# Performance work log

Measured on AMD Instinct MI355X. Metric: run time of the kernel, lower is better.

The kernel has to match this reference:

```python
import jax, jax.numpy as jnp
import numpy as np

SEQ, B, E, HID = 512, 32, 256, 256
H2 = 2 * HID              # BiLSTM output / DAG-LSTM hidden size
R, NE, NS, SW = 128, 64, 64, 8
N = NE + NS               # total node slots (entities + relation nodes)
VOCAB, NEL = 50000, 128
CLAMP_C, CLAMP_H = 100.0, 100.0


def _uni(k, shape, fan_in):
    b = 1.0 / np.sqrt(fan_in)
    return jax.random.uniform(k, shape, jnp.float32, -b, b)


def setup_inputs() -> dict:
    key = jax.random.key(0)
    ks = jax.random.split(key, 24)
    inp = {}
    inp["tokens"] = jax.random.randint(ks[0], (SEQ, B), 0, VOCAB)
    inp["entity_spans"] = jax.random.randint(ks[1], (NE, SW), 0, SEQ)
    inp["element_names"] = jax.random.randint(ks[2], (NS, B), 0, NEL)
    inp["H"] = jnp.zeros((N, B, H2), jnp.float32)
    inp["A"] = jnp.zeros((1,), jnp.int32)  # unused by forward (as in original)
    inp["T"] = jnp.broadcast_to(jnp.arange(NS, dtype=jnp.int32)[:, None] + NE, (NS, B))
    inp["S"] = jax.random.randint(ks[3], (NS, B, 2), 0, NE + 32)
    inp["entity_spans_size"] = jnp.full((B,), NE, jnp.int32)
    # learned parameters
    inp["word_emb"] = jax.random.normal(ks[4], (VOCAB, E), jnp.float32)
    inp["elem_emb"] = jax.random.normal(ks[5], (NEL, R), jnp.float32)
    inp["attn_w"] = _uni(ks[6], (1, H2), H2)
    inp["attn_b"] = _uni(ks[7], (1,), H2)
    inp["Wih_f"] = _uni(ks[8], (4 * HID, E), E)
    inp["Whh_f"] = _uni(ks[9], (4 * HID, HID), HID)
    inp["bl_f"] = _uni(ks[10], (4 * HID,), HID)
    inp["Wih_b"] = _uni(ks[11], (4 * HID, E), E)
    inp["Whh_b"] = _uni(ks[12], (4 * HID, HID), HID)
    inp["bl_b"] = _uni(ks[13], (4 * HID,), HID)
    inp["W_ioc"] = _uni(ks[14], (3 * H2, R), R + 2 * H2)
    inp["U_ioc"] = _uni(ks[15], (3 * H2, 2 * H2), R + 2 * H2)
    inp["b_ioc"] = _uni(ks[16], (3 * H2,), R + 2 * H2)
    inp["Wf"] = _uni(ks[17], (H2, R), R + H2)
    inp["Uf"] = _uni(ks[18], (H2, H2), R + H2)
    inp["bf"] = _uni(ks[19], (H2,), R + H2)
    inp["W1"] = _uni(ks[20], (2 * H2, H2), H2)
    inp["b1"] = _uni(ks[21], (2 * H2,), H2)
    inp["W2"] = _uni(ks[22], (2, 2 * H2), 2 * H2)
    inp["b2"] = _uni(ks[23], (2,), 2 * H2)
    return inp


def _lstm_dir(x, Wih, Whh, b, reverse):
    # x: [seq, batch, E]; torch gate order i, f, g, o
    h0 = jnp.zeros((x.shape[1], Whh.shape[1]), x.dtype)

    def step(carry, xt):
        h, c = carry
        g = xt @ Wih.T + h @ Whh.T + b
        i, f, gg, o = jnp.split(g, 4, axis=-1)
        c = jax.nn.sigmoid(f) * c + jax.nn.sigmoid(i) * jnp.tanh(gg)
        h = jax.nn.sigmoid(o) * jnp.tanh(c)
        return (h, c), h

    xs = x[::-1] if reverse else x
    _, hs = jax.lax.scan(step, (h0, h0), xs)
    return hs[::-1] if reverse else hs


def _forward(tokens, entity_spans, element_names, H, T, S, entity_spans_size,
             word_emb, elem_emb, attn_w, attn_b,
             Wih_f, Whh_f, bl_f, Wih_b, Whh_b, bl_b,
             W_ioc, U_ioc, b_ioc, Wf, Uf, bf, W1, b1, W2, b2):
    emb = word_emb[tokens]                                  # [SEQ,B,E]
    fwd = _lstm_dir(emb, Wih_f, Whh_f, bl_f, False)
    bwd = _lstm_dir(emb, Wih_b, Whh_b, bl_b, True)
    blstm = jnp.concatenate([fwd, bwd], axis=-1)            # [SEQ,B,H2]

    # attention pooling over entity spans; original multiplies the softmax
    # weights (which sum to 1) against blstm_out[i], so h_entity = wsum * blstm[i]
    attn = blstm @ attn_w[0] + attn_b[0]                    # [SEQ,B]
    scores = attn[entity_spans]                             # [NE,SW,B]
    wsum = jax.nn.softmax(scores, axis=1).sum(axis=1)       # [NE,B] (== 1 up to fp)
    ne = entity_spans.shape[0]
    H = H.at[:ne].set(wsum[..., None] * blstm[:ne])

    rej = jnp.array([0.999, 0.001], jnp.float32)
    acc0 = jnp.array([0.001, 0.999], jnp.float32)
    n_nodes = H.shape[0]

    def cell(hv, c, e):
        # DAG-LSTM cell: hv [2,H2] input hiddens, c [H2] shared cell state, e [R]
        ioc = e @ W_ioc.T + hv.reshape(-1) @ U_ioc.T + b_ioc
        i, o, ch = jnp.split(ioc, 3)
        f = jax.nn.sigmoid(e @ Wf.T + hv @ Uf.T + bf)       # [2,H2] per-input forget
        c_new = jnp.clip(jnp.sum(f * c[None, :], axis=0)
                         + jax.nn.sigmoid(i) * jnp.tanh(ch), -CLAMP_C, CLAMP_C)
        h = jnp.clip(jax.nn.sigmoid(o) * jnp.tanh(c_new), -CLAMP_H, CLAMP_H)
        return h, c_new

    P0 = jnp.concatenate([jnp.tile(acc0, (ne, 1)),
                          jnp.zeros((n_nodes - ne, 2), jnp.float32)], axis=0)

    def batch_body(c, xs):
        Hb, Sb, Tb, Eb, ent_sz = xs

        def step(carry, inp):
            Hb, Pb, c = carry
            args, tgt, el = inp
            valid = (tgt >= ent_sz) & (el > -1)
            cond = jnp.all(Pb[args, 1] > 0.5) & valid
            h_out, c_new = cell(Hb[args], c, elem_emb[el])
            logits = W2 @ (W1 @ h_out + b1) + b2
            pred = jnp.where(cond, jax.nn.softmax(logits), rej)
            Hb = Hb.at[tgt].set(jnp.where(cond, h_out, Hb[tgt]))
            c = jnp.where(cond, c_new, c)
            Pb = Pb.at[tgt].set(jnp.where(valid, pred, Pb[tgt]))
            return (Hb, Pb, c), None

        (Hb, Pb, c), _ = jax.lax.scan(step, (Hb, P0, c), (Sb, Tb, Eb))
        return c, Pb

    # cell state c rolls sequentially across batches, matching the torch loop order
    xs = (jnp.swapaxes(H, 0, 1), jnp.swapaxes(S, 0, 1), T.T,
          element_names.T, entity_spans_size)
    _, P = jax.lax.scan(batch_body, jnp.zeros((H.shape[-1],), jnp.float32), xs)
    return P.reshape(-1, 2)


def reference(tokens, entity_spans, element_names, H, A, T, S, entity_spans_size,
              word_emb, elem_emb, attn_w, attn_b,
              Wih_f, Whh_f, bl_f, Wih_b, Whh_b, bl_b,
              W_ioc, U_ioc, b_ioc, Wf, Uf, bf, W1, b1, W2, b2):
    return _forward(tokens, entity_spans, element_names, H, T, S, entity_spans_size,
                    word_emb, elem_emb, attn_w, attn_b,
                    Wih_f, Whh_f, bl_f, Wih_b, Whh_b, bl_b,
                    W_ioc, U_ioc, b_ioc, Wf, Uf, bf, W1, b1, W2, b2)
```

## Files before the change

kernel.cpp:

```cpp
#include <hip/hip_runtime.h>
#include <stdint.h>

#define SEQB 512
#define BATCH 32
#define EDIM 256
#define HIDN 256
#define HH2 512
#define RDIM 128
#define NEnt 64
#define NSt 64
#define NNODE 128
#define NHELP 112
#define HPG 14
#define NROWS 3584
#define TERMEVT 0xFFFFFFFFu
#define SCOPE_AGENT __HIP_MEMORY_SCOPE_AGENT

static __device__ __forceinline__ float sigm(float x) { return 1.0f / (1.0f + __expf(-x)); }
static __device__ __forceinline__ float tanh_f(float x) { return 1.0f - 2.0f / (__expf(2.0f * x) + 1.0f); }

static __device__ __forceinline__ void barrier_lds() {
  asm volatile("s_waitcnt lgkmcnt(0)" ::: "memory");
  __builtin_amdgcn_sched_barrier(0);
  __builtin_amdgcn_s_barrier();
}

template<int GATHER, int BIASFIRST>
__global__ __launch_bounds__(256) void gemm_tn(
    const float* __restrict__ A, const int* __restrict__ gidx, const float* __restrict__ gtab,
    const float* __restrict__ B0, const float* __restrict__ B1, int nsplitB,
    const float* __restrict__ bias0, const float* __restrict__ bias1, int nsplitBias,
    float* __restrict__ C, int M, int N, int K)
{
  __shared__ float As[16][132];
  __shared__ float Bs[16][132];
  const int tid = threadIdx.x;
  const int m0 = blockIdx.y * 128, n0 = blockIdx.x * 128;

  const int lrow = tid >> 1;
  const int lk   = (tid & 1) * 8;
  const float* arow;
  if (GATHER) arow = gtab + (size_t)gidx[m0 + lrow] * K + lk;
  else        arow = A + (size_t)(m0 + lrow) * K + lk;
  const int bn = n0 + lrow;
  const float* brow = ((bn < nsplitB) ? (B0 + (size_t)bn * K)
                                      : (B1 + (size_t)(bn - nsplitB) * K)) + lk;

  const int tx = tid & 15, ty = tid >> 4;

  float bb[2][4];
#pragma unroll
  for (int in = 0; in < 2; ++in)
#pragma unroll
    for (int j = 0; j < 4; ++j) bb[in][j] = 0.f;
  if (bias0) {
#pragma unroll
    for (int in = 0; in < 2; ++in)
#pragma unroll
      for (int j = 0; j < 4; ++j) {
        int n = n0 + in * 64 + tx * 4 + j;
        bb[in][j] = (n < nsplitBias) ? bias0[n] : bias1[n - nsplitBias];
      }
  }

  float acc[2][2][4][4];
#pragma unroll
  for (int im = 0; im < 2; ++im)
#pragma unroll
    for (int in = 0; in < 2; ++in)
#pragma unroll
      for (int i = 0; i < 4; ++i)
#pragma unroll
        for (int j = 0; j < 4; ++j)
          acc[im][in][i][j] = BIASFIRST ? bb[in][j] : 0.f;

  float4 pa0 = *(const float4*)(arow);
  float4 pa1 = *(const float4*)(arow + 4);
  float4 pb0 = *(const float4*)(brow);
  float4 pb1 = *(const float4*)(brow + 4);

  int k0 = 0;
  while (true) {
    __syncthreads();
    As[lk + 0][lrow] = pa0.x; As[lk + 1][lrow] = pa0.y;
    As[lk + 2][lrow] = pa0.z; As[lk + 3][lrow] = pa0.w;
    As[lk + 4][lrow] = pa1.x; As[lk + 5][lrow] = pa1.y;
    As[lk + 6][lrow] = pa1.z; As[lk + 7][lrow] = pa1.w;
    Bs[lk + 0][lrow] = pb0.x; Bs[lk + 1][lrow] = pb0.y;
    Bs[lk + 2][lrow] = pb0.z; Bs[lk + 3][lrow] = pb0.w;
    Bs[lk + 4][lrow] = pb1.x; Bs[lk + 5][lrow] = pb1.y;
    Bs[lk + 6][lrow] = pb1.z; Bs[lk + 7][lrow] = pb1.w;
    __syncthreads();

    k0 += 16;
    const bool more = (k0 < K);
    if (more) {
      pa0 = *(const float4*)(arow + k0);
      pa1 = *(const float4*)(arow + k0 + 4);
      pb0 = *(const float4*)(brow + k0);
      pb1 = *(const float4*)(brow + k0 + 4);
    }

#pragma unroll
    for (int k = 0; k < 16; ++k) {
      const float4 av0 = *(const float4*)&As[k][ty * 4];
      const float4 av1 = *(const float4*)&As[k][64 + ty * 4];
      const float4 bv0 = *(const float4*)&Bs[k][tx * 4];
      const float4 bv1 = *(const float4*)&Bs[k][64 + tx * 4];
      const float am[2][4] = {{av0.x, av0.y, av0.z, av0.w},
                              {av1.x, av1.y, av1.z, av1.w}};
      const float bw[2][4] = {{bv0.x, bv0.y, bv0.z, bv0.w},
                              {bv1.x, bv1.y, bv1.z, bv1.w}};
#pragma unroll
      for (int im = 0; im < 2; ++im)
#pragma unroll
        for (int in = 0; in < 2; ++in)
#pragma unroll
          for (int i = 0; i < 4; ++i)
#pragma unroll
            for (int j = 0; j < 4; ++j)
              acc[im][in][i][j] += am[im][i] * bw[in][j];
    }
    if (!more) break;
  }

#pragma unroll
  for (int im = 0; im < 2; ++im)
#pragma unroll
    for (int i = 0; i < 4; ++i) {
      const int m = m0 + im * 64 + ty * 4 + i;
#pragma unroll
      for (int in = 0; in < 2; ++in) {
        float4 o;
        o.x = acc[im][in][i][0] + (BIASFIRST ? 0.f : bb[in][0]);
        o.y = acc[im][in][i][1] + (BIASFIRST ? 0.f : bb[in][1]);
        o.z = acc[im][in][i][2] + (BIASFIRST ? 0.f : bb[in][2]);
        o.w = acc[im][in][i][3] + (BIASFIRST ? 0.f : bb[in][3]);
        *(float4*)&C[(size_t)m * N + n0 + in * 64 + tx * 4] = o;
      }
    }
}

__global__ __launch_bounds__(256, 1) void lstm_esplit(
    const float* __restrict__ Xg,
    const float* __restrict__ Whh_f, const float* __restrict__ Whh_b,
    unsigned long long* __restrict__ hxbuf,
    float* __restrict__ blstm)
{
  const int tid = threadIdx.x;
  const int pid = blockIdx.x;
  const int q = pid >> 6, chain = pid & 63;
  const int d = chain >> 5, b = chain & 31;
  const int j = tid & 63;
  const int g = tid >> 6;
  const int elem = q * 64 + j;
  const int grow = g * 256 + elem;

  const float* W = (d ? Whh_b : Whh_f) + (size_t)grow * 256;
  float4 w4[64];
#pragma unroll
  for (int i = 0; i < 64; ++i) w4[i] = *(const float4*)(W + 4 * i);

  __shared__ float h_lds[HIDN];
  __shared__ float gsL[256];
  float creg = 0.f;
  h_lds[tid] = 0.f;
  __syncthreads();

  const float4* h4 = (const float4*)h_lds;
  const int pe = (tid < q * 64) ? tid : (tid + 64);
  const size_t xgoff = (size_t)d * 1024 + grow;

  for (int it = 0; it < SEQB; ++it) {
    const int t = d ? (SEQB - 1 - it) : it;
    const size_t m = (size_t)t * BATCH + b;
    const float xv = Xg[m * 2048 + xgoff];

    if (tid < 192) {
      const unsigned long long* src =
          &hxbuf[((size_t)(it & 1) * 64 + chain) * 256 + pe];
      unsigned long long qv;
      do { qv = __hip_atomic_load(src, __ATOMIC_RELAXED, SCOPE_AGENT); }
      while ((unsigned)(qv >> 32) != (unsigned)it);
      h_lds[pe] = __uint_as_float((unsigned)qv);
    }
    barrier_lds();

    float a0 = 0.f, a1 = 0.f, a2 = 0.f, a3 = 0.f;
#pragma unroll
    for (int i = 0; i < 64; ++i) {
      const float4 hv = h4[i];
      const float4 wv = w4[i];
      a0 += wv.x * hv.x; a1 += wv.y * hv.y; a2 += wv.z * hv.z; a3 += wv.w * hv.w;
    }
    gsL[tid] = (a0 + a1) + (a2 + a3) + xv;
    barrier_lds();

    if (tid < 64) {
      const float gi = gsL[tid], gf = gsL[64 + tid];
      const float gg = gsL[128 + tid], go = gsL[192 + tid];
      creg = sigm(gf) * creg + sigm(gi) * tanh_f(gg);
      const float hn = sigm(go) * tanh_f(creg);
      h_lds[elem] = hn;
      const unsigned long long pk =
          ((unsigned long long)(unsigned)(it + 1) << 32) |
          (unsigned long long)__float_as_uint(hn);
      __hip_atomic_store(&hxbuf[((size_t)((it + 1) & 1) * 64 + chain) * 256 + elem], pk,
                         __ATOMIC_RELAXED, SCOPE_AGENT);
      blstm[m * HH2 + (size_t)d * HIDN + elem] = hn;
    }
    barrier_lds();
  }
}

__global__ __launch_bounds__(256) void attn_k(const float* __restrict__ blstm,
                                              const float* __restrict__ attn_w,
                                              const float* __restrict__ attn_b,
                                              float* __restrict__ attnv)
{
  const int tid = threadIdx.x;
  const int p = blockIdx.x * 4 + (tid >> 6);
  const int lane = tid & 63;
  const size_t base = (size_t)p * HH2 + lane * 8;
  float4 v0 = *(const float4*)&blstm[base];
  float4 v1 = *(const float4*)&blstm[base + 4];
  float4 w0 = *(const float4*)&attn_w[lane * 8];
  float4 w1 = *(const float4*)&attn_w[lane * 8 + 4];
  float acc = v0.x * w0.x + v0.y * w0.y + v0.z * w0.z + v0.w * w0.w
            + v1.x * w1.x + v1.y * w1.y + v1.z * w1.z + v1.w * w1.w;
#pragma unroll
  for (int off = 32; off > 0; off >>= 1) acc += __shfl_down(acc, off);
  if (lane == 0) attnv[p] = acc + attn_b[0];
}

__global__ __launch_bounds__(64) void entity_prep(const int* __restrict__ spans,
                                                  const float* __restrict__ attnv,
                                                  const float* __restrict__ blstm,
                                                  float* __restrict__ Hent,
                                                  float* __restrict__ P_out)
{
  const int nb = blockIdx.x;
  const int n = nb >> 5, b = nb & 31;
  const int tid = threadIdx.x;
  __shared__ float sc[8];
  if (tid < 8) sc[tid] = attnv[spans[n * 8 + tid] * BATCH + b];
  __syncthreads();
  float mx = sc[0];
#pragma unroll
  for (int w = 1; w < 8; ++w) mx = fmaxf(mx, sc[w]);
  float ex[8]; float ssum = 0.f;
#pragma unroll
  for (int w = 0; w < 8; ++w) { ex[w] = __expf(sc[w] - mx); ssum += ex[w]; }
  float wsum = 0.f;
#pragma unroll
  for (int w = 0; w < 8; ++w) wsum += ex[w] / ssum;
  const size_t base = ((size_t)n * BATCH + b) * HH2;
#pragma unroll
  for (int q = 0; q < 2; ++q) {
    int j = q * 256 + tid * 4;
    float4 v = *(const float4*)&blstm[base + j];
    v.x *= wsum; v.y *= wsum; v.z *= wsum; v.w *= wsum;
    *(float4*)&Hent[base + j] = v;
  }
  if (tid == 0) {
    P_out[((size_t)b * NNODE + n) * 2 + 0] = 0.001f;
    P_out[((size_t)b * NNODE + n) * 2 + 1] = 0.999f;
  }
}

__global__ void pack_ucat(const float* __restrict__ U_ioc, const float* __restrict__ Uf,
                          float* __restrict__ Ucat)
{
  int j = blockIdx.x, tid = threadIdx.x;
  for (int k = tid; k < 512; k += 128) {
    float v;
    if (j < 1536)      v = U_ioc[(size_t)j * 1024 + k];
    else if (j < 3072) v = U_ioc[(size_t)(j - 1536) * 1024 + 512 + k];
    else               v = Uf[(size_t)(j - 3072) * 512 + k];
    Ucat[(size_t)j * 512 + k] = v;
  }
}

__global__ __launch_bounds__(256) void mprep(const float* __restrict__ W1,
                                             const float* __restrict__ b1,
                                             const float* __restrict__ W2,
                                             const float* __restrict__ b2,
                                             float* __restrict__ Mmat,
                                             float* __restrict__ mbv)
{
  const int tid = threadIdx.x;
  for (int j = tid; j < 512; j += 256) {
    float a0 = 0.f, a1 = 0.f;
    for (int m = 0; m < 1024; ++m) {
      float w = W1[(size_t)m * 512 + j];
      a0 += W2[m] * w;
      a1 += W2[1024 + m] * w;
    }
    Mmat[j] = a0; Mmat[512 + j] = a1;
  }
  if (tid < 2) {
    float a = b2[tid];
    for (int m = 0; m < 1024; ++m) a += W2[tid * 1024 + m] * b1[m];
    mbv[tid] = a;
  }
}

__global__ __launch_bounds__(512) void dag_seq(
    const int* __restrict__ S, const int* __restrict__ T, const int* __restrict__ EN,
    const int* __restrict__ entsz,
    const float* __restrict__ WE,
    const float* __restrict__ Mmat, const float* __restrict__ mbv,
    float* __restrict__ Tall, float* __restrict__ hbuf,
    uint32_t* head, uint32_t* slotbase, uint32_t* arrive,
    const float* __restrict__ Ucat, float* __restrict__ P_out)
{
  const int tid = threadIdx.x;
  __shared__ int   SL[NSt * BATCH * 2];
  __shared__ int   TLt[NSt * BATCH];
  __shared__ int   ELt[NSt * BATCH];
  __shared__ int   eszL[BATCH];
  __shared__ float MmatL[1024];
  __shared__ float mbvL[2];
  __shared__ float pstL[NNODE];
  __shared__ int   evtofL[NSt];
  __shared__ int   confL[NSt];
  __shared__ float red0[2][8], red1[2][8];
  __shared__ uint32_t sslot;

  if (blockIdx.x < NHELP) {
    const int w = blockIdx.x;
    const int row = w * 32 + (tid >> 4);
    const int ks = (tid & 15) * 32;
    float wreg[32];
#pragma unroll
    for (int i = 0; i < 8; ++i) {
      float4 v = *(const float4*)&Ucat[(size_t)row * 512 + ks + i * 4];
      wreg[i * 4 + 0] = v.x; wreg[i * 4 + 1] = v.y; wreg[i * 4 + 2] = v.z; wreg[i * 4 + 3] = v.w;
    }
    uint32_t done = 0;
    const int g = w & 7;
    while (true) {
      if (tid == 0) {
        while (__hip_atomic_load(head, __ATOMIC_RELAXED, SCOPE_AGENT) <= done) {
          __builtin_amdgcn_s_sleep(4);
        }
        __builtin_amdgcn_fence(__ATOMIC_ACQUIRE, "agent");
        sslot = slotbase[done];
      }
      __syncthreads();
      const uint32_t slot = sslot;
      if (slot == TERMEVT) break;
      const float* hv = hbuf + (size_t)done * HH2 + ks;
      float acc = 0.f;
#pragma unroll
      for (int i = 0; i < 8; ++i) {
        float4 v = *(const float4*)&hv[i * 4];
        acc += wreg[i * 4 + 0] * v.x + wreg[i * 4 + 1] * v.y
             + wreg[i * 4 + 2] * v.z + wreg[i * 4 + 3] * v.w;
      }
      acc += __shfl_down(acc, 8);
      acc += __shfl_down(acc, 4);
      acc += __shfl_down(acc, 2);
      acc += __shfl_down(acc, 1);
      if ((tid & 15) == 0) {
        __hip_atomic_store(&Tall[(size_t)slot + row], acc, __ATOMIC_RELAXED, SCOPE_AGENT);
      }
      __syncthreads();
      if (tid == 0) {
        __hip_atomic_fetch_add(&arrive[done * 8 + g], 1u, __ATOMIC_RELEASE, SCOPE_AGENT);
      }
      ++done;
    }
    return;
  }

  for (int i = tid; i < NSt * BATCH * 2; i += 512) SL[i] = S[i];
  for (int i = tid; i < NSt * BATCH; i += 512) { TLt[i] = T[i]; ELt[i] = EN[i]; }
  for (int i = tid; i < 1024; i += 512) MmatL[i] = Mmat[i];
  if (tid < BATCH) eszL[tid] = entsz[tid];
  if (tid < 2) mbvL[tid] = mbv[tid];
  __syncthreads();

  float c = 0.f;
  uint32_t e = 0;
  for (int b = 0; b < BATCH; ++b) {
    barrier_lds();
    const int esz = eszL[b];
    for (int j = tid; j < NNODE; j += 512) pstL[j] = (j < NEnt) ? 0.999f : 0.f;
    if (tid < NSt) { confL[tid] = 0; evtofL[tid] = -1; }
    __syncthreads();
    int fp = 0;

    bool  pfok = false;
    float pt0 = 0.f, pt1 = 0.f, pt2 = 0.f, pt3 = 0.f, pt4 = 0.f, pt5 = 0.f, pt6 = 0.f, pt7 = 0.f;
    float pw0 = 0.f, pw1 = 0.f, pw2 = 0.f, pwf = 0.f;

#define PFETCH(sn)                                                              \
    do {                                                                        \
      pfok = false;                                                             \
      if ((sn) < NSt) {                                                         \
        const int sbn_ = (sn) * BATCH + b;                                      \
        const int na0_ = SL[2 * sbn_], na1_ = SL[2 * sbn_ + 1];                 \
        const int nel_ = ELt[sbn_];                                             \
        if (nel_ >= 0) {                                                        \
          const float* nwe_ = WE + (size_t)nel_ * 2048;                         \
          pw0 = nwe_[tid]; pw1 = nwe_[512 + tid]; pw2 = nwe_[1024 + tid];       \
          pwf = nwe_[1536 + tid];                                               \
        }                                                                       \
        const bool ok0_ = (na0_ < NEnt) || (confL[na0_ - NEnt] != 0);           \
        const bool ok1_ = (na1_ < NEnt) || (confL[na1_ - NEnt] != 0);           \
        if (ok0_ && ok1_) {                                                     \
          const size_t ns0_ = ((size_t)na0_ * BATCH + b) * NROWS;               \
          const size_t ns1_ = ((size_t)na1_ * BATCH + b) * NROWS;               \
          pt0 = Tall[ns0_ + tid];               pt1 = Tall[ns1_ + 1536 + tid];  \
          pt2 = Tall[ns0_ + 512 + tid];         pt3 = Tall[ns1_ + 2048 + tid];  \
          pt4 = Tall[ns0_ + 1024 + tid];        pt5 = Tall[ns1_ + 2560 + tid];  \
          pt6 = Tall[ns0_ + 3072 + tid];        pt7 = Tall[ns1_ + 3072 + tid];  \
          pfok = true;                                                          \
        }                                                                       \
      }                                                                         \
    } while (0)

    PFETCH(0);

    for (int s = 0; s < NSt; ++s) {
      const int sb = s * BATCH + b;
      const int a0 = SL[2 * sb], a1 = SL[2 * sb + 1];
      const int tgt = TLt[sb], el = ELt[sb];
      const bool valid = (tgt >= esz) && (el > -1);
      const float pa0 = pstL[a0], pa1 = pstL[a1];
      const bool cond = valid && (pa0 > 0.5f) && (pa1 > 0.5f);
      if (cond) {
        if (!pfok) {
          const int r0 = (a0 >= NEnt) ? (a0 - NEnt) : -1;
          const int r1 = (a1 >= NEnt) ? (a1 - NEnt) : -1;
          if (tid < 8 && r0 >= 0 && !confL[r0]) {
            const uint32_t ev = (uint32_t)evtofL[r0];
            while (__hip_atomic_load(&arrive[ev * 8 + tid], __ATOMIC_RELAXED, SCOPE_AGENT)
                   < (uint32_t)HPG) { __builtin_amdgcn_s_sleep(1); }
          }
          if (tid >= 8 && tid < 16 && r1 >= 0 && !confL[r1]) {
            const uint32_t ev = (uint32_t)evtofL[r1];
            while (__hip_atomic_load(&arrive[ev * 8 + (tid - 8)], __ATOMIC_RELAXED, SCOPE_AGENT)
                   < (uint32_t)HPG) { __builtin_amdgcn_s_sleep(1); }
          }
          __syncthreads();
          if (tid == 0) {
            __builtin_amdgcn_fence(__ATOMIC_ACQUIRE, "agent");
            int evm = -1;
            if (r0 >= 0) { confL[r0] = 1; if (evtofL[r0] > evm) evm = evtofL[r0]; }
            if (r1 >= 0) { confL[r1] = 1; if (evtofL[r1] > evm) evm = evtofL[r1]; }
            if (evm >= 0) {
              for (int r = 0; r < 32; ++r) {
                const int ev_ = evtofL[r];
                if (ev_ >= 0 && ev_ <= evm) confL[r] = 1;
              }
            }
          }
          __syncthreads();
          const size_t s0 = ((size_t)a0 * BATCH + b) * NROWS;
          const size_t s1 = ((size_t)a1 * BATCH + b) * NROWS;
          pt0 = Tall[s0 + tid];        pt1 = Tall[s1 + 1536 + tid];
          pt2 = Tall[s0 + 512 + tid];  pt3 = Tall[s1 + 2048 + tid];
          pt4 = Tall[s0 + 1024 + tid]; pt5 = Tall[s1 + 2560 + tid];
          pt6 = Tall[s0 + 3072 + tid]; pt7 = Tall[s1 + 3072 + tid];
        }
        const float ii = pw0 + pt0 + pt1;
        const float oo = pw1 + pt2 + pt3;
        const float ch = pw2 + pt4 + pt5;
        const float f0 = sigm(pwf + pt6);
        const float f1 = sigm(pwf + pt7);
        PFETCH(s + 1);
        float cn = (f0 + f1) * c + sigm(ii) * tanh_f(ch);
        cn = fminf(fmaxf(cn, -100.f), 100.f);
        float hh = sigm(oo) * tanh_f(cn);
        hh = fminf(fmaxf(hh, -100.f), 100.f);
        float l0 = MmatL[tid] * hh, l1 = MmatL[512 + tid] * hh;
#pragma unroll
        for (int off = 32; off > 0; off >>= 1) {
          l0 += __shfl_down(l0, off);
          l1 += __shfl_down(l1, off);
        }
        if ((tid & 63) == 0) { red0[fp][tid >> 6] = l0; red1[fp][tid >> 6] = l1; }
        barrier_lds();
        float L0 = mbvL[0], L1 = mbvL[1];
#pragma unroll
        for (int wv = 0; wv < 8; ++wv) { L0 += red0[fp][wv]; L1 += red1[fp][wv]; }
        const float mx = fmaxf(L0, L1);
        const float e0 = __expf(L0 - mx), e1 = __expf(L1 - mx);
        const float inv = 1.f / (e0 + e1);
        const float o0 = e0 * inv, o1 = e1 * inv;
        if ((tid & 63) == 0) pstL[tgt] = o1;
        if (tid == 0) {
          P_out[((size_t)b * NNODE + tgt) * 2 + 0] = o0;
          P_out[((size_t)b * NNODE + tgt) * 2 + 1] = o1;
        }
        fp ^= 1;
        c = cn;
        const bool pub = (o1 > 0.5f) && (tgt < NEnt + 32);
        if (pub) {
          __hip_atomic_store(&hbuf[(size_t)e * HH2 + tid], hh, __ATOMIC_RELAXED, SCOPE_AGENT);
          __syncthreads();
          if (tid == 0) {
            evtofL[tgt - NEnt] = (int)e;
            __hip_atomic_store(&slotbase[e], (uint32_t)(((uint32_t)tgt * BATCH + (uint32_t)b) * NROWS),
                               __ATOMIC_RELAXED, SCOPE_AGENT);
            __hip_atomic_store(head, e + 1u, __ATOMIC_RELEASE, SCOPE_AGENT);
          }
          ++e;
          barrier_lds();
        }
      } else {
        PFETCH(s + 1);
        if (tid == 0 && (valid || tgt >= NEnt)) {
          const float o0 = valid ? 0.999f : ((tgt < NEnt) ? 0.001f : 0.f);
          const float o1 = valid ? 0.001f : ((tgt < NEnt) ? 0.999f : 0.f);
          P_out[((size_t)b * NNODE + tgt) * 2 + 0] = o0;
          P_out[((size_t)b * NNODE + tgt) * 2 + 1] = o1;
        }
        if (valid && (tid & 63) == 0) pstL[tgt] = 0.001f;
      }
    }
#undef PFETCH
  }
  if (tid == 0) {
    __hip_atomic_store(&slotbase[e], TERMEVT, __ATOMIC_RELAXED, SCOPE_AGENT);
    __hip_atomic_store(head, e + 1u, __ATOMIC_RELEASE, SCOPE_AGENT);
  }
}

extern "C" void kernel_launch(void* const* d_in, const int* in_sizes, int n_in,
                              void* d_out, int out_size, void* d_ws, size_t ws_size,
                              hipStream_t stream)
{
  const int* tokens = (const int*)d_in[0];
  const int* spans  = (const int*)d_in[1];
  const int* enames = (const int*)d_in[2];
  const int* T      = (const int*)d_in[5];
  const int* S      = (const int*)d_in[6];
  const int* entsz  = (const int*)d_in[7];
  const float* word_emb = (const float*)d_in[8];
  const float* elem_emb = (const float*)d_in[9];
  const float* attn_w = (const float*)d_in[10];
  const float* attn_b = (const float*)d_in[11];
  const float* Wih_f = (const float*)d_in[12];
  const float* Whh_f = (const float*)d_in[13];
  const float* bl_f  = (const float*)d_in[14];
  const float* Wih_b = (const float*)d_in[15];
  const float* Whh_b = (const float*)d_in[16];
  const float* bl_b  = (const float*)d_in[17];
  const float* W_ioc = (const float*)d_in[18];
  const float* U_ioc = (const float*)d_in[19];
  const float* b_ioc = (const float*)d_in[20];
  const float* Wf    = (const float*)d_in[21];
  const float* Uf    = (const float*)d_in[22];
  const float* bf    = (const float*)d_in[23];
  const float* W1    = (const float*)d_in[24];
  const float* b1    = (const float*)d_in[25];
  const float* W2    = (const float*)d_in[26];
  const float* b2    = (const float*)d_in[27];
  float* P_out = (float*)d_out;

  char* ws = (char*)d_ws;
  uint32_t* head     = (uint32_t*)ws;
  uint32_t* slotbase = (uint32_t*)(ws + 8192);
  uint32_t* arrive   = (uint32_t*)(ws + 16384);
  float* fws = (float*)(ws + 65536);
  size_t off = 0;
  float* Xg    = fws + off; off += (size_t)16384 * 2048;
  float* blstm = fws + off; off += (size_t)SEQB * BATCH * HH2;
  float* attnv = fws + off; off += (size_t)SEQB * BATCH;
  float* Hent  = fws + off; off += (size_t)2048 * 512;
  float* Tall  = fws + off; off += (size_t)96 * BATCH * NROWS;
  unsigned long long* hxbuf = (unsigned long long*)(fws + off);
  off += (size_t)2 * 64 * 256 * 2;
  float* Ucat  = fws + off; off += (size_t)NROWS * 512;
  float* WE    = fws + off; off += (size_t)128 * 2048;
  float* Mmat  = fws + off; off += 1024;
  float* mbv   = fws + off; off += 16;
  float* hbuf  = fws + off; off += (size_t)1024 * 512;
  const size_t needed = 65536 + off * sizeof(float);
  if (ws_size < needed) return;

  hipMemsetAsync(d_ws, 0, 65536, stream);
  hipMemsetAsync(hxbuf, 0, (size_t)2 * 64 * 256 * 8, stream);

  gemm_tn<1, 0><<<dim3(2048 / 128, 16384 / 128), 256, 0, stream>>>(
      nullptr, tokens, word_emb, Wih_f, Wih_b, 1024, bl_f, bl_b, 1024,
      Xg, 16384, 2048, 256);

  lstm_esplit<<<256, 256, 0, stream>>>(Xg, Whh_f, Whh_b, hxbuf, blstm);

  attn_k<<<4096, 256, 0, stream>>>(blstm, attn_w, attn_b, attnv);
  entity_prep<<<2048, 64, 0, stream>>>(spans, attnv, blstm, Hent, P_out);

  pack_ucat<<<NROWS, 128, 0, stream>>>(U_ioc, Uf, Ucat);
  gemm_tn<0, 1><<<dim3(2048 / 128, 1), 256, 0, stream>>>(
      elem_emb, nullptr, nullptr, W_ioc, Wf, 1536, b_ioc, bf, 1536,
      WE, 128, 2048, 128);
  mprep<<<1, 256, 0, stream>>>(W1, b1, W2, b2, Mmat, mbv);
  gemm_tn<0, 0><<<dim3(NROWS / 128, 2048 / 128), 256, 0, stream>>>(
      Hent, nullptr, nullptr, Ucat, nullptr, 0x40000000, nullptr, nullptr, 0,
      Tall, 2048, NROWS, 512);

  dag_seq<<<NHELP + 1, 512, 0, stream>>>(S, T, enames, entsz, WE, Mmat, mbv,
                                         Tall, hbuf, head, slotbase, arrive, Ucat, P_out);
}
```

Before: 5.462 ms.

## Use tagged hot buffer and packed head to cut producer-consumer sync latency

Helper blocks now write each projected row as a 64-bit value tagged with the event number into a double-buffered hot array. The sequential block polls those tags directly when it needs the most recent event, instead of waiting on arrive counters and then re-reading Tall. The slot is packed into a 64-bit head word so helpers skip the slotbase read, and the hbuf store and wave-level arrive increments are moved earlier to shorten the critical path. This adds heavier polling traffic and subtle memory-ordering assumptions about tag visibility and buffer reuse.

```diff
diff --git a/kernel.cpp b/kernel.cpp
--- a/kernel.cpp
+++ b/kernel.cpp
@@ -12,6 +12,7 @@
 #define NNODE 128
 #define NHELP 112
 #define HPG 14
+#define HPW 112
 #define NROWS 3584
 #define TERMEVT 0xFFFFFFFFu
 #define SCOPE_AGENT __HIP_MEMORY_SCOPE_AGENT
@@ -311,7 +312,8 @@
     const float* __restrict__ WE,
     const float* __restrict__ Mmat, const float* __restrict__ mbv,
     float* __restrict__ Tall, float* __restrict__ hbuf,
-    uint32_t* head, uint32_t* slotbase, uint32_t* arrive,
+    unsigned long long* head64, uint32_t* slotbase, uint32_t* arrive,
+    unsigned long long* hotT,
     const float* __restrict__ Ucat, float* __restrict__ P_out)
 {
   const int tid = threadIdx.x;
@@ -341,11 +343,11 @@
     const int g = w & 7;
     while (true) {
       if (tid == 0) {
-        while (__hip_atomic_load(head, __ATOMIC_RELAXED, SCOPE_AGENT) <= done) {
-          __builtin_amdgcn_s_sleep(4);
-        }
+        unsigned long long hq;
+        while ((uint32_t)((hq = __hip_atomic_load(head64, __ATOMIC_RELAXED, SCOPE_AGENT)) >> 32)
+               <= done) { __builtin_amdgcn_s_sleep(1); }
         __builtin_amdgcn_fence(__ATOMIC_ACQUIRE, "agent");
-        sslot = slotbase[done];
+        sslot = ((uint32_t)(hq >> 32) == done + 1u) ? (uint32_t)hq : slotbase[done];
       }
       __syncthreads();
       const uint32_t slot = sslot;
@@ -364,9 +366,13 @@
       acc += __shfl_down(acc, 1);
       if ((tid & 15) == 0) {
         __hip_atomic_store(&Tall[(size_t)slot + row], acc, __ATOMIC_RELAXED, SCOPE_AGENT);
+        const unsigned long long hq =
+            ((unsigned long long)(done + 1u) << 32) |
+            (unsigned long long)__float_as_uint(acc);
+        __hip_atomic_store(&hotT[(size_t)(done & 1u) * NROWS + row], hq,
+                           __ATOMIC_RELAXED, SCOPE_AGENT);
       }
-      __syncthreads();
-      if (tid == 0) {
+      if ((tid & 63) == 0) {
         __hip_atomic_fetch_add(&arrive[done * 8 + g], 1u, __ATOMIC_RELEASE, SCOPE_AGENT);
       }
       ++done;
@@ -421,6 +427,23 @@
       }                                                                         \
     } while (0)
 
+#define HOTPOLL4(rA, rB, rC, rD, dA, dB, dC, dD)                                \
+    do {                                                                        \
+      const unsigned long long* hp_ = hotT + (size_t)par_ * NROWS;              \
+      unsigned long long qa_, qb_, qc_, qd_;                                    \
+      for (;;) {                                                                \
+        qa_ = __hip_atomic_load(hp_ + (rA), __ATOMIC_RELAXED, SCOPE_AGENT);     \
+        qb_ = __hip_atomic_load(hp_ + (rB), __ATOMIC_RELAXED, SCOPE_AGENT);     \
+        qc_ = __hip_atomic_load(hp_ + (rC), __ATOMIC_RELAXED, SCOPE_AGENT);     \
+        qd_ = __hip_atomic_load(hp_ + (rD), __ATOMIC_RELAXED, SCOPE_AGENT);     \
+        if ((((uint32_t)(qa_ >> 32)) == etag_) & (((uint32_t)(qb_ >> 32)) == etag_) & \
+            (((uint32_t)(qc_ >> 32)) == etag_) & (((uint32_t)(qd_ >> 32)) == etag_))  \
+          break;                                                                \
+      }                                                                         \
+      dA = __uint_as_float((uint32_t)qa_); dB = __uint_as_float((uint32_t)qb_); \
+      dC = __uint_as_float((uint32_t)qc_); dD = __uint_as_float((uint32_t)qd_); \
+    } while (0)
+
     PFETCH(0);
 
     for (int s = 0; s < NSt; ++s) {
@@ -434,47 +457,68 @@
         if (!pfok) {
           const int r0 = (a0 >= NEnt) ? (a0 - NEnt) : -1;
           const int r1 = (a1 >= NEnt) ? (a1 - NEnt) : -1;
-          if (tid < 8 && r0 >= 0 && !confL[r0]) {
-            const uint32_t ev = (uint32_t)evtofL[r0];
-            while (__hip_atomic_load(&arrive[ev * 8 + tid], __ATOMIC_RELAXED, SCOPE_AGENT)
-                   < (uint32_t)HPG) { __builtin_amdgcn_s_sleep(1); }
-          }
-          if (tid >= 8 && tid < 16 && r1 >= 0 && !confL[r1]) {
-            const uint32_t ev = (uint32_t)evtofL[r1];
-            while (__hip_atomic_load(&arrive[ev * 8 + (tid - 8)], __ATOMIC_RELAXED, SCOPE_AGENT)
-                   < (uint32_t)HPG) { __builtin_amdgcn_s_sleep(1); }
-          }
-          __syncthreads();
-          if (tid == 0) {
-            __builtin_amdgcn_fence(__ATOMIC_ACQUIRE, "agent");
-            int evm = -1;
-            if (r0 >= 0) { confL[r0] = 1; if (evtofL[r0] > evm) evm = evtofL[r0]; }
-            if (r1 >= 0) { confL[r1] = 1; if (evtofL[r1] > evm) evm = evtofL[r1]; }
-            if (evm >= 0) {
-              for (int r = 0; r < 32; ++r) {
-                const int ev_ = evtofL[r];
-                if (ev_ >= 0 && ev_ <= evm) confL[r] = 1;
+          const bool c0ok = (r0 < 0) || (confL[r0] != 0);
+          const bool c1ok = (r1 < 0) || (confL[r1] != 0);
+          const bool f0 = !c0ok && (evtofL[r0] == (int)e - 1);
+          const bool f1 = !c1ok && (evtofL[r1] == (int)e - 1);
+          const bool w0 = !c0ok && !f0;
+          const bool w1 = !c1ok && !f1;
+          if (w0 || w1) {
+            if (tid < 8 && w0) {
+              const uint32_t ev = (uint32_t)evtofL[r0];
+              while (__hip_atomic_load(&arrive[ev * 8 + tid], __ATOMIC_RELAXED, SCOPE_AGENT)
+                     < (uint32_t)HPW) { __builtin_amdgcn_s_sleep(1); }
+            }
+            if (tid >= 8 && tid < 16 && w1) {
+              const uint32_t ev = (uint32_t)evtofL[r1];
+              while (__hip_atomic_load(&arrive[ev * 8 + (tid - 8)], __ATOMIC_RELAXED, SCOPE_AGENT)
+                     < (uint32_t)HPW) { __builtin_amdgcn_s_sleep(1); }
+            }
+            __syncthreads();
+            if (tid == 0) {
+              __builtin_amdgcn_fence(__ATOMIC_ACQUIRE, "agent");
+              int evm = -1;
+              if (w0) { confL[r0] = 1; if (evtofL[r0] > evm) evm = evtofL[r0]; }
+              if (w1) { confL[r1] = 1; if (evtofL[r1] > evm) evm = evtofL[r1]; }
+              if (evm >= 0) {
+                for (int r = 0; r < 32; ++r) {
+                  const int ev_ = evtofL[r];
+                  if (ev_ >= 0 && ev_ <= evm) confL[r] = 1;
+                }
               }
             }
+            __syncthreads();
           }
-          __syncthreads();
           const size_t s0 = ((size_t)a0 * BATCH + b) * NROWS;
           const size_t s1 = ((size_t)a1 * BATCH + b) * NROWS;
-          pt0 = Tall[s0 + tid];        pt1 = Tall[s1 + 1536 + tid];
-          pt2 = Tall[s0 + 512 + tid];  pt3 = Tall[s1 + 2048 + tid];
-          pt4 = Tall[s0 + 1024 + tid]; pt5 = Tall[s1 + 2560 + tid];
-          pt6 = Tall[s0 + 3072 + tid]; pt7 = Tall[s1 + 3072 + tid];
+          const int par_ = (int)((e - 1u) & 1u);
+          const uint32_t etag_ = (uint32_t)e;
+          if (f0) {
+            HOTPOLL4(tid, 512 + tid, 1024 + tid, 3072 + tid, pt0, pt2, pt4, pt6);
+          } else {
+            pt0 = Tall[s0 + tid];        pt2 = Tall[s0 + 512 + tid];
+            pt4 = Tall[s0 + 1024 + tid]; pt6 = Tall[s0 + 3072 + tid];
+          }
+          if (f1) {
+            HOTPOLL4(1536 + tid, 2048 + tid, 2560 + tid, 3072 + tid, pt1, pt3, pt5, pt7);
+          } else {
+            pt1 = Tall[s1 + 1536 + tid]; pt3 = Tall[s1 + 2048 + tid];
+            pt5 = Tall[s1 + 2560 + tid]; pt7 = Tall[s1 + 3072 + tid];
+          }
         }
         const float ii = pw0 + pt0 + pt1;
         const float oo = pw1 + pt2 + pt3;
         const float ch = pw2 + pt4 + pt5;
-        const float f0 = sigm(pwf + pt6);
-        const float f1 = sigm(pwf + pt7);
+        const float f0g = sigm(pwf + pt6);
+        const float f1g = sigm(pwf + pt7);
         PFETCH(s + 1);
-        float cn = (f0 + f1) * c + sigm(ii) * tanh_f(ch);
+        float cn = (f0g + f1g) * c + sigm(ii) * tanh_f(ch);
         cn = fminf(fmaxf(cn, -100.f), 100.f);
         float hh = sigm(oo) * tanh_f(cn);
         hh = fminf(fmaxf(hh, -100.f), 100.f);
+        if (tgt < NEnt + 32) {
+          __hip_atomic_store(&hbuf[(size_t)e * HH2 + tid], hh, __ATOMIC_RELAXED, SCOPE_AGENT);
+        }
         float l0 = MmatL[tid] * hh, l1 = MmatL[512 + tid] * hh;
 #pragma unroll
         for (int off = 32; off > 0; off >>= 1) {
@@ -499,13 +543,14 @@
         c = cn;
         const bool pub = (o1 > 0.5f) && (tgt < NEnt + 32);
         if (pub) {
-          __hip_atomic_store(&hbuf[(size_t)e * HH2 + tid], hh, __ATOMIC_RELAXED, SCOPE_AGENT);
           __syncthreads();
           if (tid == 0) {
             evtofL[tgt - NEnt] = (int)e;
-            __hip_atomic_store(&slotbase[e], (uint32_t)(((uint32_t)tgt * BATCH + (uint32_t)b) * NROWS),
-                               __ATOMIC_RELAXED, SCOPE_AGENT);
-            __hip_atomic_store(head, e + 1u, __ATOMIC_RELEASE, SCOPE_AGENT);
+            const uint32_t slot = (uint32_t)(((uint32_t)tgt * BATCH + (uint32_t)b) * NROWS);
+            __hip_atomic_store(&slotbase[e], slot, __ATOMIC_RELAXED, SCOPE_AGENT);
+            __hip_atomic_store(head64,
+                               ((unsigned long long)(e + 1u) << 32) | (unsigned long long)slot,
+                               __ATOMIC_RELEASE, SCOPE_AGENT);
           }
           ++e;
           barrier_lds();
@@ -522,10 +567,13 @@
       }
     }
 #undef PFETCH
+#undef HOTPOLL4
   }
   if (tid == 0) {
     __hip_atomic_store(&slotbase[e], TERMEVT, __ATOMIC_RELAXED, SCOPE_AGENT);
-    __hip_atomic_store(head, e + 1u, __ATOMIC_RELEASE, SCOPE_AGENT);
+    __hip_atomic_store(head64,
+                       ((unsigned long long)(e + 1u) << 32) | (unsigned long long)TERMEVT,
+                       __ATOMIC_RELEASE, SCOPE_AGENT);
   }
 }
 
@@ -562,10 +610,11 @@
   float* P_out = (float*)d_out;
 
   char* ws = (char*)d_ws;
-  uint32_t* head     = (uint32_t*)ws;
+  unsigned long long* head64 = (unsigned long long*)ws;
   uint32_t* slotbase = (uint32_t*)(ws + 8192);
   uint32_t* arrive   = (uint32_t*)(ws + 16384);
-  float* fws = (float*)(ws + 65536);
+  unsigned long long* hotT = (unsigned long long*)(ws + 49152);
+  float* fws = (float*)(ws + 131072);
   size_t off = 0;
   float* Xg    = fws + off; off += (size_t)16384 * 2048;
   float* blstm = fws + off; off += (size_t)SEQB * BATCH * HH2;
@@ -579,10 +628,10 @@
   float* Mmat  = fws + off; off += 1024;
   float* mbv   = fws + off; off += 16;
   float* hbuf  = fws + off; off += (size_t)1024 * 512;
-  const size_t needed = 65536 + off * sizeof(float);
+  const size_t needed = 131072 + off * sizeof(float);
   if (ws_size < needed) return;
 
-  hipMemsetAsync(d_ws, 0, 65536, stream);
+  hipMemsetAsync(d_ws, 0, 131072, stream);
   hipMemsetAsync(hxbuf, 0, (size_t)2 * 64 * 256 * 8, stream);
 
   gemm_tn<1, 0><<<dim3(2048 / 128, 16384 / 128), 256, 0, stream>>>(
@@ -604,5 +653,6 @@
       Tall, 2048, NROWS, 512);
 
   dag_seq<<<NHELP + 1, 512, 0, stream>>>(S, T, enames, entsz, WE, Mmat, mbv,
-                                         Tall, hbuf, head, slotbase, arrive, Ucat, P_out);
-}
+                                         Tall, hbuf, head64, slotbase, arrive, hotT,
+                                         Ucat, P_out);
+}
```

After: 7.906 ms. 1.45x slower.

## Publish DAG hidden state before softmax and poll slot array instead of head

Applied to the files above, without the earlier changes.

Drops the separate head counter: helper blocks now poll slotbase[done] directly for a nonzero entry, and the producer writes that slot with release ordering. Each relation-node hidden state is now published before the output softmax reduction rather than after it, and without the o1>0.5 check. This lets the helper GEMVs overlap with the classifier reduction and removes one atomic handoff per event. The cost is that helpers run a GEMV for every candidate node, not only accepted ones. The scheme also relies on slotbase being zero-initialised, since any nonzero value is treated as a published slot.

```diff
diff --git a/kernel.cpp b/kernel.cpp
--- a/kernel.cpp
+++ b/kernel.cpp
@@ -311,7 +311,7 @@
     const float* __restrict__ WE,
     const float* __restrict__ Mmat, const float* __restrict__ mbv,
     float* __restrict__ Tall, float* __restrict__ hbuf,
-    uint32_t* head, uint32_t* slotbase, uint32_t* arrive,
+    uint32_t* slotbase, uint32_t* arrive,
     const float* __restrict__ Ucat, float* __restrict__ P_out)
 {
   const int tid = threadIdx.x;
@@ -341,11 +341,12 @@
     const int g = w & 7;
     while (true) {
       if (tid == 0) {
-        while (__hip_atomic_load(head, __ATOMIC_RELAXED, SCOPE_AGENT) <= done) {
-          __builtin_amdgcn_s_sleep(4);
+        uint32_t sv;
+        while ((sv = __hip_atomic_load(&slotbase[done], __ATOMIC_RELAXED, SCOPE_AGENT)) == 0u) {
+          __builtin_amdgcn_s_sleep(1);
         }
         __builtin_amdgcn_fence(__ATOMIC_ACQUIRE, "agent");
-        sslot = slotbase[done];
+        sslot = sv;
       }
       __syncthreads();
       const uint32_t slot = sslot;
@@ -448,8 +449,8 @@
           if (tid == 0) {
             __builtin_amdgcn_fence(__ATOMIC_ACQUIRE, "agent");
             int evm = -1;
-            if (r0 >= 0) { confL[r0] = 1; if (evtofL[r0] > evm) evm = evtofL[r0]; }
-            if (r1 >= 0) { confL[r1] = 1; if (evtofL[r1] > evm) evm = evtofL[r1]; }
+            if (r0 >= 0 && !confL[r0]) { confL[r0] = 1; if (evtofL[r0] > evm) evm = evtofL[r0]; }
+            if (r1 >= 0 && !confL[r1]) { confL[r1] = 1; if (evtofL[r1] > evm) evm = evtofL[r1]; }
             if (evm >= 0) {
               for (int r = 0; r < 32; ++r) {
                 const int ev_ = evtofL[r];
@@ -468,13 +469,17 @@
         const float ii = pw0 + pt0 + pt1;
         const float oo = pw1 + pt2 + pt3;
         const float ch = pw2 + pt4 + pt5;
-        const float f0 = sigm(pwf + pt6);
-        const float f1 = sigm(pwf + pt7);
+        const float f0g = sigm(pwf + pt6);
+        const float f1g = sigm(pwf + pt7);
         PFETCH(s + 1);
-        float cn = (f0 + f1) * c + sigm(ii) * tanh_f(ch);
+        float cn = (f0g + f1g) * c + sigm(ii) * tanh_f(ch);
         cn = fminf(fmaxf(cn, -100.f), 100.f);
         float hh = sigm(oo) * tanh_f(cn);
         hh = fminf(fmaxf(hh, -100.f), 100.f);
+        const bool pubc = (tgt < NEnt + 32);
+        if (pubc) {
+          __hip_atomic_store(&hbuf[(size_t)e * HH2 + tid], hh, __ATOMIC_RELAXED, SCOPE_AGENT);
+        }
         float l0 = MmatL[tid] * hh, l1 = MmatL[512 + tid] * hh;
 #pragma unroll
         for (int off = 32; off > 0; off >>= 1) {
@@ -482,7 +487,17 @@
           l1 += __shfl_down(l1, off);
         }
         if ((tid & 63) == 0) { red0[fp][tid >> 6] = l0; red1[fp][tid >> 6] = l1; }
-        barrier_lds();
+        if (pubc) {
+          __syncthreads();
+          if (tid == 0) {
+            evtofL[tgt - NEnt] = (int)e;
+            __hip_atomic_store(&slotbase[e],
+                               (uint32_t)(((uint32_t)tgt * BATCH + (uint32_t)b) * NROWS),
+                               __ATOMIC_RELEASE, SCOPE_AGENT);
+          }
+        } else {
+          barrier_lds();
+        }
         float L0 = mbvL[0], L1 = mbvL[1];
 #pragma unroll
         for (int wv = 0; wv < 8; ++wv) { L0 += red0[fp][wv]; L1 += red1[fp][wv]; }
@@ -497,16 +512,7 @@
         }
         fp ^= 1;
         c = cn;
-        const bool pub = (o1 > 0.5f) && (tgt < NEnt + 32);
-        if (pub) {
-          __hip_atomic_store(&hbuf[(size_t)e * HH2 + tid], hh, __ATOMIC_RELAXED, SCOPE_AGENT);
-          __syncthreads();
-          if (tid == 0) {
-            evtofL[tgt - NEnt] = (int)e;
-            __hip_atomic_store(&slotbase[e], (uint32_t)(((uint32_t)tgt * BATCH + (uint32_t)b) * NROWS),
-                               __ATOMIC_RELAXED, SCOPE_AGENT);
-            __hip_atomic_store(head, e + 1u, __ATOMIC_RELEASE, SCOPE_AGENT);
-          }
+        if (pubc) {
           ++e;
           barrier_lds();
         }
@@ -524,8 +530,7 @@
 #undef PFETCH
   }
   if (tid == 0) {
-    __hip_atomic_store(&slotbase[e], TERMEVT, __ATOMIC_RELAXED, SCOPE_AGENT);
-    __hip_atomic_store(head, e + 1u, __ATOMIC_RELEASE, SCOPE_AGENT);
+    __hip_atomic_store(&slotbase[e], TERMEVT, __ATOMIC_RELEASE, SCOPE_AGENT);
   }
 }
 
@@ -562,7 +567,6 @@
   float* P_out = (float*)d_out;
 
   char* ws = (char*)d_ws;
-  uint32_t* head     = (uint32_t*)ws;
   uint32_t* slotbase = (uint32_t*)(ws + 8192);
   uint32_t* arrive   = (uint32_t*)(ws + 16384);
   float* fws = (float*)(ws + 65536);
@@ -604,5 +608,5 @@
       Tall, 2048, NROWS, 512);
 
   dag_seq<<<NHELP + 1, 512, 0, stream>>>(S, T, enames, entsz, WE, Mmat, mbv,
-                                         Tall, hbuf, head, slotbase, arrive, Ucat, P_out);
-}
+                                         Tall, hbuf, slotbase, arrive, Ucat, P_out);
+}
```

New measurement: 5.497 ms. No clear change (+0.6%).
